# Optimization experiments

Measured on AMD Instinct MI355X. Metric: run time of the kernel, lower is better.

## Reference

```python
import jax, jax.numpy as jnp
import numpy as np

B, F, HIST, FUT, L = 512, 1024, 20, 30, 3


def setup_inputs() -> dict:
    key = jax.random.key(0)
    k0, k1, k2 = jax.random.split(key, 3)
    # xavier_normal with gain 0.9 for [4F, F] weights: std = gain*sqrt(2/(fan_in+fan_out))
    std = 0.9 * np.sqrt(2.0 / (4 * F + F)).astype(np.float32)
    seq_input = jax.random.normal(k0, (B, F, HIST), jnp.float32)
    Wih = jax.random.normal(k1, (L, 4 * F, F), jnp.float32) * std
    Whh = jax.random.normal(k2, (L, 4 * F, F), jnp.float32) * std
    bih = jnp.zeros((L, 4 * F), jnp.float32)
    bhh = jnp.zeros((L, 4 * F), jnp.float32)
    return {"seq_input": seq_input, "Wih": Wih, "Whh": Whh,
            "bih": bih, "bhh": bhh, "fut_len": FUT}


def _lstm_cell(x, h, c, Wih, Whh, bih, bhh):
    # torch.nn.LSTMCell math, gate order i, f, g, o
    gates = x @ Wih.T + bih + h @ Whh.T + bhh  # [B, 4F]
    i, f, g, o = jnp.split(gates, 4, axis=-1)
    c_new = jax.nn.sigmoid(f) * c + jax.nn.sigmoid(i) * jnp.tanh(g)
    h_new = jax.nn.sigmoid(o) * jnp.tanh(c_new)
    return h_new, c_new


def _stack_step(h, c, x, Wih, Whh, bih, bhh):
    # h, c: [L, B, F]; x: [B, F]. Python loop over L=3 layers only.
    nL = Wih.shape[0]
    hs, cs = [], []
    inp = x
    for l in range(nL):
        h_l, c_l = _lstm_cell(inp, h[l], c[l], Wih[l], Whh[l], bih[l], bhh[l])
        hs.append(h_l)
        cs.append(c_l)
        inp = h_l
    return jnp.stack(hs), jnp.stack(cs)


def reference(seq_input, Wih, Whh, bih, bhh, fut_len):
    b, f, _ = seq_input.shape
    nL = Wih.shape[0]
    h0 = jnp.zeros((nL, b, f), seq_input.dtype)
    c0 = jnp.zeros((nL, b, f), seq_input.dtype)
    xs = jnp.transpose(seq_input, (2, 0, 1))  # [hist_len, B, F]

    def hist_step(carry, x):
        h, c = carry
        h, c = _stack_step(h, c, x, Wih, Whh, bih, bhh)
        return (h, c), None

    (h, c), _ = jax.lax.scan(hist_step, (h0, c0), xs)

    def fut_step(carry, _):
        h, c, x = carry
        h, c = _stack_step(h, c, x, Wih, Whh, bih, bhh)
        y = h[-1]  # recurrent_input = top-layer hidden state
        return (h, c, y), y

    # first decoder input is the top-layer CELL state after history
    _, ys = jax.lax.scan(fut_step, (h, c, c[-1]), None, length=fut_len)
    return jnp.transpose(ys, (1, 2, 0))  # [B, F, fut_len]
```

## Files before the change

kernel.cpp:

```cpp
#include <hip/hip_runtime.h>


#define BDIM 512
#define FDIM 1024
#define HISTLEN 20
#define LAYERS 3
#define NG 4096
#define KD 1024

typedef __attribute__((ext_vector_type(8))) short short8;
typedef __attribute__((ext_vector_type(4))) float f32x4;

__device__ __forceinline__ float sigf(float x) { return 1.f / (1.f + __expf(-x)); }
__device__ __forceinline__ float tanh_fast(float x) {
    float e = __expf(-2.f * fabsf(x));
    float r = (1.f - e) / (1.f + e);
    return copysignf(r, x);
}
__device__ __forceinline__ ushort bfhi(float w) { return (ushort)(__float_as_uint(w) >> 16); }
__device__ __forceinline__ float hif(float w) { return __uint_as_float(__float_as_uint(w) & 0xFFFF0000u); }
__device__ __forceinline__ ushort bflo(float w) { return bfhi(w - hif(w)); }

constexpr int LDT = 40;

__global__ __launch_bounds__(256, 2) void gemm_split(
    const ushort* __restrict__ A0hi, const ushort* __restrict__ A0lo,
    const float*  __restrict__ W0,
    const ushort* __restrict__ A1hi, const ushort* __restrict__ A1lo,
    const float*  __restrict__ W1,
    float* __restrict__ gp)
{
    __shared__ __attribute__((aligned(16))) ushort WhiL[128 * LDT];
    __shared__ __attribute__((aligned(16))) ushort WloL[128 * LDT];
    __shared__ __attribute__((aligned(16))) ushort AhiL[128 * LDT];
    __shared__ __attribute__((aligned(16))) ushort AloL[128 * LDT];

    const int z  = blockIdx.z;
    const int s  = z & 1;
    const int kh = z >> 1;
    const ushort* Ahi = s ? A1hi : A0hi;
    const ushort* Alo = s ? A1lo : A0lo;
    const float*  W   = s ? W1 : W0;
    float*        out = gp + (size_t)z * BDIM * NG;

    const int tid = threadIdx.x;
    const int m0 = blockIdx.y * 128;
    const int n0 = blockIdx.x * 128;

    const int srow  = tid >> 1;
    const int shalf = tid & 1;
    const int s_lds = srow * LDT + shalf * 16;

    const int lane = tid & 63;
    const int wid  = tid >> 6;
    const int wm = (wid & 1) * 64;
    const int wn = (wid >> 1) * 64;
    const int frow = lane & 15;
    const int oct  = lane >> 4;

    int a_off[4], w_off[4];
    #pragma unroll
    for (int i = 0; i < 4; ++i) {
        a_off[i] = (wm + i * 16 + frow) * LDT + oct * 8;
        w_off[i] = (wn + i * 16 + frow) * LDT + oct * 8;
    }

    f32x4 acc[4][4] = {};

    const float*  wg_base = W   + (size_t)(n0 + srow) * KD + shalf * 16;
    const ushort* ah_base = Ahi + (size_t)(m0 + srow) * KD + shalf * 16;
    const ushort* al_base = Alo + (size_t)(m0 + srow) * KD + shalf * 16;

    const int kbeg = kh * (KD / 2);
    const int kend = kbeg + KD / 2;

    for (int k0 = kbeg; k0 < kend; k0 += 32) {
        float4 w4[4];
        #pragma unroll
        for (int q = 0; q < 4; ++q) w4[q] = *(const float4*)(wg_base + k0 + q * 4);
        short8 ah0 = *(const short8*)(ah_base + k0);
        short8 ah1 = *(const short8*)(ah_base + k0 + 8);
        short8 al0 = *(const short8*)(al_base + k0);
        short8 al1 = *(const short8*)(al_base + k0 + 8);

        ushort whi[16], wlo[16];
        #pragma unroll
        for (int e = 0; e < 16; ++e) {
            float w = ((const float*)w4)[e];
            unsigned u = __float_as_uint(w);
            whi[e] = (ushort)(u >> 16);
            float r = w - __uint_as_float(u & 0xFFFF0000u);
            wlo[e] = (ushort)(__float_as_uint(r) >> 16);
        }

        __syncthreads();
        *(short8*)&WhiL[s_lds]     = *(short8*)&whi[0];
        *(short8*)&WhiL[s_lds + 8] = *(short8*)&whi[8];
        *(short8*)&WloL[s_lds]     = *(short8*)&wlo[0];
        *(short8*)&WloL[s_lds + 8] = *(short8*)&wlo[8];
        *(short8*)&AhiL[s_lds]     = ah0;
        *(short8*)&AhiL[s_lds + 8] = ah1;
        *(short8*)&AloL[s_lds]     = al0;
        *(short8*)&AloL[s_lds + 8] = al1;
        __syncthreads();

        short8 fa_hi[4], fa_lo[4];
        #pragma unroll
        for (int i = 0; i < 4; ++i) {
            fa_hi[i] = *(const short8*)&AhiL[a_off[i]];
            fa_lo[i] = *(const short8*)&AloL[a_off[i]];
        }
        #pragma unroll
        for (int j = 0; j < 4; ++j) {
            short8 fb_hi = *(const short8*)&WhiL[w_off[j]];
            short8 fb_lo = *(const short8*)&WloL[w_off[j]];
            #pragma unroll
            for (int i = 0; i < 4; ++i) {
                acc[i][j] = __builtin_amdgcn_mfma_f32_16x16x32_bf16(fa_hi[i], fb_hi, acc[i][j], 0, 0, 0);
                acc[i][j] = __builtin_amdgcn_mfma_f32_16x16x32_bf16(fa_lo[i], fb_hi, acc[i][j], 0, 0, 0);
                acc[i][j] = __builtin_amdgcn_mfma_f32_16x16x32_bf16(fa_hi[i], fb_lo, acc[i][j], 0, 0, 0);
            }
        }
    }

    #pragma unroll
    for (int i = 0; i < 4; ++i) {
        #pragma unroll
        for (int j = 0; j < 4; ++j) {
            int col = n0 + wn + j * 16 + frow;
            #pragma unroll
            for (int r = 0; r < 4; ++r) {
                int row = m0 + wm + i * 16 + oct * 4 + r;
                out[(size_t)row * NG + col] = acc[i][j][r];
            }
        }
    }
}

__global__ void cell_fuse(const float* __restrict__ gp,
                          const float* __restrict__ bi, const float* __restrict__ bh,
                          float* __restrict__ c,
                          ushort* __restrict__ Hhi, ushort* __restrict__ Hlo,
                          float* __restrict__ y, int t, int fut)
{
    const size_t MN = (size_t)BDIM * NG;
    int idx = blockIdx.x * blockDim.x + threadIdx.x;
    int b = idx >> 10, f = idx & 1023;
    const float* g0 = gp + (size_t)b * NG;
    const float* g1 = g0 + MN;
    const float* g2 = g1 + MN;
    const float* g3 = g2 + MN;
    float ig = g0[f] + g1[f] + g2[f] + g3[f] + bi[f] + bh[f];
    float fg = g0[FDIM + f] + g1[FDIM + f] + g2[FDIM + f] + g3[FDIM + f]
             + bi[FDIM + f] + bh[FDIM + f];
    float gg = g0[2 * FDIM + f] + g1[2 * FDIM + f] + g2[2 * FDIM + f] + g3[2 * FDIM + f]
             + bi[2 * FDIM + f] + bh[2 * FDIM + f];
    float og = g0[3 * FDIM + f] + g1[3 * FDIM + f] + g2[3 * FDIM + f] + g3[3 * FDIM + f]
             + bi[3 * FDIM + f] + bh[3 * FDIM + f];
    float cn = sigf(fg) * c[idx] + sigf(ig) * tanh_fast(gg);
    float hn = sigf(og) * tanh_fast(cn);
    c[idx] = cn;
    Hhi[idx] = bfhi(hn);
    Hlo[idx] = bflo(hn);
    if (y) y[(size_t)idx * fut + t] = hn;
}

__global__ void pack_split(const float* __restrict__ seq,
                           ushort* __restrict__ Xhi, ushort* __restrict__ Xlo, int t)
{
    int idx = blockIdx.x * blockDim.x + threadIdx.x;
    float v = seq[(size_t)idx * HISTLEN + t];
    Xhi[idx] = bfhi(v);
    Xlo[idx] = bflo(v);
}

__global__ void split_vec(const float* __restrict__ src,
                          ushort* __restrict__ hi, ushort* __restrict__ lo)
{
    int idx = blockIdx.x * blockDim.x + threadIdx.x;
    float v = src[idx];
    hi[idx] = bfhi(v);
    lo[idx] = bflo(v);
}

extern "C" void kernel_launch(void* const* d_in, const int* in_sizes, int n_in,
                              void* d_out, int out_size, void* d_ws, size_t ws_size,
                              hipStream_t stream)
{
    const float* seq = (const float*)d_in[0];
    const float* Wih = (const float*)d_in[1];
    const float* Whh = (const float*)d_in[2];
    const float* bih = (const float*)d_in[3];
    const float* bhh = (const float*)d_in[4];
    float* out = (float*)d_out;

    const int fut = out_size / (BDIM * FDIM);
    const size_t BF = (size_t)BDIM * FDIM;
    const size_t Wsz = (size_t)NG * KD;
    const size_t MN  = (size_t)BDIM * NG;

    float*  c   = (float*)d_ws;
    ushort* Hhi = (ushort*)(c + LAYERS * BF);
    ushort* Hlo = Hhi + LAYERS * BF;
    ushort* Xhi = Hlo + LAYERS * BF;
    ushort* Xlo = Xhi + BF;
    float*  gp  = (float*)(Xlo + BF);

    hipMemsetAsync(d_ws, 0, LAYERS * BF * 8, stream);

    dim3 ggrid(NG / 128, BDIM / 128, 4);
    const int cgrid = (int)(BF / 256);

    for (int t = 0; t < HISTLEN + fut; ++t) {
        const bool dec = (t >= HISTLEN);
        if (!dec) {
            pack_split<<<cgrid, 256, 0, stream>>>(seq, Xhi, Xlo, t);
        } else if (t == HISTLEN) {
            split_vec<<<cgrid, 256, 0, stream>>>(c + 2 * BF, Xhi, Xlo);
        }
        for (int l = 0; l < LAYERS; ++l) {
            const ushort* axh;
            const ushort* axl;
            if (l > 0)        { axh = Hhi + (size_t)(l - 1) * BF; axl = Hlo + (size_t)(l - 1) * BF; }
            else if (!dec || t == HISTLEN) { axh = Xhi; axl = Xlo; }
            else              { axh = Hhi + 2 * BF; axl = Hlo + 2 * BF; }

            gemm_split<<<ggrid, 256, 0, stream>>>(
                axh, axl, Wih + (size_t)l * Wsz,
                Hhi + (size_t)l * BF, Hlo + (size_t)l * BF, Whh + (size_t)l * Wsz,
                gp);

            cell_fuse<<<cgrid, 256, 0, stream>>>(
                gp, bih + l * NG, bhh + l * NG,
                c + (size_t)l * BF, Hhi + (size_t)l * BF, Hlo + (size_t)l * BF,
                (dec && l == LAYERS - 1) ? out : nullptr, dec ? t - HISTLEN : 0, fut);
        }
    }
}
```

Before: 6.505 ms.

## Pre-split weights to bf16 hi/lo once and double-buffer GEMM via direct-to-LDS loads

Adds a one-time prep kernel that splits the fp32 weights into bf16 hi/lo arrays in the workspace, so the per-step GEMM no longer reloads fp32 weights and redoes the conversion. The GEMM stages its tiles with global_load_lds straight into a double-buffered, XOR-swizzled LDS layout. Explicit vmcnt waits and barriers let the next K-tile load overlap the MFMA work on the current one, and setprio raises wave priority during the MFMA section. This costs extra workspace and a prep pass on every call, and the launch returns early without doing anything if the workspace is too small.

```diff
diff --git a/kernel.cpp b/kernel.cpp
--- a/kernel.cpp
+++ b/kernel.cpp
@@ -7,9 +7,11 @@
 #define LAYERS 3
 #define NG 4096
 #define KD 1024
+#define KSTEPS 16
 
 typedef __attribute__((ext_vector_type(8))) short short8;
 typedef __attribute__((ext_vector_type(4))) float f32x4;
+typedef __attribute__((ext_vector_type(4))) unsigned short u16x4;
 
 __device__ __forceinline__ float sigf(float x) { return 1.f / (1.f + __expf(-x)); }
 __device__ __forceinline__ float tanh_fast(float x) {
@@ -21,35 +23,66 @@
 __device__ __forceinline__ float hif(float w) { return __uint_as_float(__float_as_uint(w) & 0xFFFF0000u); }
 __device__ __forceinline__ ushort bflo(float w) { return bfhi(w - hif(w)); }
 
-constexpr int LDT = 40;
+__device__ __forceinline__ void gl16(const ushort* g, ushort* l) {
+    __builtin_amdgcn_global_load_lds(
+        (const __attribute__((address_space(1))) unsigned int*)g,
+        (__attribute__((address_space(3))) unsigned int*)l, 16, 0, 0);
+}
+
+__global__ void prep_w(const float* __restrict__ Wih, const float* __restrict__ Whh,
+                       ushort* __restrict__ Whi, ushort* __restrict__ Wlo)
+{
+    size_t i4 = ((size_t)blockIdx.x * 256 + threadIdx.x) * 4;
+    size_t slot = i4 >> 22;
+    size_t off  = i4 & 0x3FFFFFu;
+    const float* src = ((slot & 1) ? Whh : Wih) + ((slot >> 1) << 22) + off;
+    float4 v = *(const float4*)src;
+    u16x4 hi, lo;
+    #pragma unroll
+    for (int e = 0; e < 4; ++e) {
+        float w = ((const float*)&v)[e];
+        unsigned u = __float_as_uint(w);
+        hi[e] = (ushort)(u >> 16);
+        float r = w - __uint_as_float(u & 0xFFFF0000u);
+        lo[e] = (ushort)(__float_as_uint(r) >> 16);
+    }
+    *(u16x4*)(Whi + i4) = hi;
+    *(u16x4*)(Wlo + i4) = lo;
+}
 
 __global__ __launch_bounds__(256, 2) void gemm_split(
     const ushort* __restrict__ A0hi, const ushort* __restrict__ A0lo,
-    const float*  __restrict__ W0,
+    const ushort* __restrict__ W0hi, const ushort* __restrict__ W0lo,
     const ushort* __restrict__ A1hi, const ushort* __restrict__ A1lo,
-    const float*  __restrict__ W1,
+    const ushort* __restrict__ W1hi, const ushort* __restrict__ W1lo,
     float* __restrict__ gp)
 {
-    __shared__ __attribute__((aligned(16))) ushort WhiL[128 * LDT];
-    __shared__ __attribute__((aligned(16))) ushort WloL[128 * LDT];
-    __shared__ __attribute__((aligned(16))) ushort AhiL[128 * LDT];
-    __shared__ __attribute__((aligned(16))) ushort AloL[128 * LDT];
+    __shared__ __attribute__((aligned(16))) ushort lds[2][4][4096];
 
     const int z  = blockIdx.z;
     const int s  = z & 1;
     const int kh = z >> 1;
     const ushort* Ahi = s ? A1hi : A0hi;
     const ushort* Alo = s ? A1lo : A0lo;
-    const float*  W   = s ? W1 : W0;
-    float*        out = gp + (size_t)z * BDIM * NG;
+    const ushort* Whi = s ? W1hi : W0hi;
+    const ushort* Wlo = s ? W1lo : W0lo;
+    float* out = gp + (size_t)z * BDIM * NG;
 
     const int tid = threadIdx.x;
     const int m0 = blockIdx.y * 128;
     const int n0 = blockIdx.x * 128;
 
-    const int srow  = tid >> 1;
-    const int shalf = tid & 1;
-    const int s_lds = srow * LDT + shalf * 16;
+    const int srow = tid >> 2;
+    const int sc   = tid & 3;
+    const int sf   = (srow >> 1) & 3;
+    const int scol = (sc ^ sf) << 3;
+    const int kbeg = kh * (KD / 2);
+
+    const ushort* pAhi = Ahi + (size_t)(m0 + srow) * KD + kbeg + scol;
+    const ushort* pAlo = Alo + (size_t)(m0 + srow) * KD + kbeg + scol;
+    const ushort* pWhi = Whi + (size_t)(n0 + srow) * KD + kbeg + scol;
+    const ushort* pWlo = Wlo + (size_t)(n0 + srow) * KD + kbeg + scol;
+    const int rstep = 64 * KD;
 
     const int lane = tid & 63;
     const int wid  = tid >> 6;
@@ -58,70 +91,69 @@
     const int frow = lane & 15;
     const int oct  = lane >> 4;
 
-    int a_off[4], w_off[4];
+    int a_e[4], w_e[4];
     #pragma unroll
     for (int i = 0; i < 4; ++i) {
-        a_off[i] = (wm + i * 16 + frow) * LDT + oct * 8;
-        w_off[i] = (wn + i * 16 + frow) * LDT + oct * 8;
+        int ra = wm + i * 16 + frow;
+        a_e[i] = ra * 32 + (((oct ^ (ra >> 1)) & 3) << 3);
+        int rw = wn + i * 16 + frow;
+        w_e[i] = rw * 32 + (((oct ^ (rw >> 1)) & 3) << 3);
     }
 
     f32x4 acc[4][4] = {};
 
-    const float*  wg_base = W   + (size_t)(n0 + srow) * KD + shalf * 16;
-    const ushort* ah_base = Ahi + (size_t)(m0 + srow) * KD + shalf * 16;
-    const ushort* al_base = Alo + (size_t)(m0 + srow) * KD + shalf * 16;
-
-    const int kbeg = kh * (KD / 2);
-    const int kend = kbeg + KD / 2;
-
-    for (int k0 = kbeg; k0 < kend; k0 += 32) {
-        float4 w4[4];
-        #pragma unroll
-        for (int q = 0; q < 4; ++q) w4[q] = *(const float4*)(wg_base + k0 + q * 4);
-        short8 ah0 = *(const short8*)(ah_base + k0);
-        short8 ah1 = *(const short8*)(ah_base + k0 + 8);
-        short8 al0 = *(const short8*)(al_base + k0);
-        short8 al1 = *(const short8*)(al_base + k0 + 8);
-
-        ushort whi[16], wlo[16];
-        #pragma unroll
-        for (int e = 0; e < 16; ++e) {
-            float w = ((const float*)w4)[e];
-            unsigned u = __float_as_uint(w);
-            whi[e] = (ushort)(u >> 16);
-            float r = w - __uint_as_float(u & 0xFFFF0000u);
-            wlo[e] = (ushort)(__float_as_uint(r) >> 16);
-        }
-
-        __syncthreads();
-        *(short8*)&WhiL[s_lds]     = *(short8*)&whi[0];
-        *(short8*)&WhiL[s_lds + 8] = *(short8*)&whi[8];
-        *(short8*)&WloL[s_lds]     = *(short8*)&wlo[0];
-        *(short8*)&WloL[s_lds + 8] = *(short8*)&wlo[8];
-        *(short8*)&AhiL[s_lds]     = ah0;
-        *(short8*)&AhiL[s_lds + 8] = ah1;
-        *(short8*)&AloL[s_lds]     = al0;
-        *(short8*)&AloL[s_lds + 8] = al1;
-        __syncthreads();
-
-        short8 fa_hi[4], fa_lo[4];
+    auto STAGE = [&](ushort* buf, int kk) {
+        ushort* d0 = buf + tid * 8;
+        gl16(pAhi + kk,         d0);
+        gl16(pAlo + kk,         d0 + 4096);
+        gl16(pWhi + kk,         d0 + 8192);
+        gl16(pWlo + kk,         d0 + 12288);
+        ushort* d1 = d0 + 2048;
+        gl16(pAhi + rstep + kk, d1);
+        gl16(pAlo + rstep + kk, d1 + 4096);
+        gl16(pWhi + rstep + kk, d1 + 8192);
+        gl16(pWlo + rstep + kk, d1 + 12288);
+    };
+
+    auto COMPUTE = [&](const ushort* buf) {
+        short8 fah[4], fal[4], fbh[4], fbl[4];
         #pragma unroll
         for (int i = 0; i < 4; ++i) {
-            fa_hi[i] = *(const short8*)&AhiL[a_off[i]];
-            fa_lo[i] = *(const short8*)&AloL[a_off[i]];
-        }
+            fah[i] = *(const short8*)(buf + a_e[i]);
+            fal[i] = *(const short8*)(buf + 4096 + a_e[i]);
+            fbh[i] = *(const short8*)(buf + 8192 + w_e[i]);
+            fbl[i] = *(const short8*)(buf + 12288 + w_e[i]);
+        }
+        asm volatile("s_waitcnt lgkmcnt(0)" ::: "memory");
+        __builtin_amdgcn_sched_barrier(0);
+        __builtin_amdgcn_s_barrier();
+        __builtin_amdgcn_sched_barrier(0);
+        __builtin_amdgcn_s_setprio(1);
         #pragma unroll
         for (int j = 0; j < 4; ++j) {
-            short8 fb_hi = *(const short8*)&WhiL[w_off[j]];
-            short8 fb_lo = *(const short8*)&WloL[w_off[j]];
             #pragma unroll
             for (int i = 0; i < 4; ++i) {
-                acc[i][j] = __builtin_amdgcn_mfma_f32_16x16x32_bf16(fa_hi[i], fb_hi, acc[i][j], 0, 0, 0);
-                acc[i][j] = __builtin_amdgcn_mfma_f32_16x16x32_bf16(fa_lo[i], fb_hi, acc[i][j], 0, 0, 0);
-                acc[i][j] = __builtin_amdgcn_mfma_f32_16x16x32_bf16(fa_hi[i], fb_lo, acc[i][j], 0, 0, 0);
+                acc[i][j] = __builtin_amdgcn_mfma_f32_16x16x32_bf16(fah[i], fbh[j], acc[i][j], 0, 0, 0);
+                acc[i][j] = __builtin_amdgcn_mfma_f32_16x16x32_bf16(fal[i], fbh[j], acc[i][j], 0, 0, 0);
+                acc[i][j] = __builtin_amdgcn_mfma_f32_16x16x32_bf16(fah[i], fbl[j], acc[i][j], 0, 0, 0);
             }
         }
-    }
+        __builtin_amdgcn_s_setprio(0);
+    };
+
+    STAGE(&lds[0][0][0], 0);
+    #pragma unroll 1
+    for (int t = 0; t < KSTEPS - 1; ++t) {
+        STAGE(&lds[(t + 1) & 1][0][0], (t + 1) * 32);
+        asm volatile("s_waitcnt vmcnt(8)" ::: "memory");
+        __builtin_amdgcn_sched_barrier(0);
+        __builtin_amdgcn_s_barrier();
+        __builtin_amdgcn_sched_barrier(0);
+        COMPUTE(&lds[t & 1][0][0]);
+    }
+    asm volatile("s_waitcnt vmcnt(0)" ::: "memory");
+    __builtin_amdgcn_s_barrier();
+    COMPUTE(&lds[(KSTEPS - 1) & 1][0][0]);
 
     #pragma unroll
     for (int i = 0; i < 4; ++i) {
@@ -196,8 +228,8 @@
 
     const int fut = out_size / (BDIM * FDIM);
     const size_t BF = (size_t)BDIM * FDIM;
-    const size_t Wsz = (size_t)NG * KD;
-    const size_t MN  = (size_t)BDIM * NG;
+    const size_t MN = (size_t)BDIM * NG;
+    const size_t Wsl = (size_t)1 << 22;
 
     float*  c   = (float*)d_ws;
     ushort* Hhi = (ushort*)(c + LAYERS * BF);
@@ -205,8 +237,14 @@
     ushort* Xhi = Hlo + LAYERS * BF;
     ushort* Xlo = Xhi + BF;
     float*  gp  = (float*)(Xlo + BF);
+    ushort* Whi = (ushort*)(gp + 4 * MN);
+    ushort* Wlo = Whi + 6 * Wsl;
+
+    const size_t need = (size_t)((char*)(Wlo + 6 * Wsl) - (char*)d_ws);
+    if (ws_size < need) return;
 
     hipMemsetAsync(d_ws, 0, LAYERS * BF * 8, stream);
+    prep_w<<<24576, 256, 0, stream>>>(Wih, Whh, Whi, Wlo);
 
     dim3 ggrid(NG / 128, BDIM / 128, 4);
     const int cgrid = (int)(BF / 256);
@@ -226,8 +264,9 @@
             else              { axh = Hhi + 2 * BF; axl = Hlo + 2 * BF; }
 
             gemm_split<<<ggrid, 256, 0, stream>>>(
-                axh, axl, Wih + (size_t)l * Wsz,
-                Hhi + (size_t)l * BF, Hlo + (size_t)l * BF, Whh + (size_t)l * Wsz,
+                axh, axl, Whi + (size_t)(2 * l) * Wsl, Wlo + (size_t)(2 * l) * Wsl,
+                Hhi + (size_t)l * BF, Hlo + (size_t)l * BF,
+                Whi + (size_t)(2 * l + 1) * Wsl, Wlo + (size_t)(2 * l + 1) * Wsl,
                 gp);
 
             cell_fuse<<<cgrid, 256, 0, stream>>>(
```

Result: faster. 5.827 ms (-10.4%).
